# Performance work log

Measured on AMD Instinct MI355X. Metric: run time of the kernel, lower is better.

## Reference

```python
import jax, jax.numpy as jnp
import numpy as np

N_NODES = 50000
N_EDGES = 800000
D = 256


def gcn_conv(x, edge_index, W, b, n_nodes):
    """PyG-style GCNConv: add self-loops, symmetric norm, linear, scatter-add."""
    # add self loops
    loops = jnp.arange(n_nodes, dtype=edge_index.dtype)
    src = jnp.concatenate([edge_index[0], loops])  # message sources
    dst = jnp.concatenate([edge_index[1], loops])  # aggregation targets
    # symmetric normalization: deg computed on targets (incl. self loops)
    deg = jax.ops.segment_sum(jnp.ones_like(dst, dtype=x.dtype), dst,
                              num_segments=n_nodes)
    dinv = jnp.where(deg > 0, jax.lax.rsqrt(deg), 0.0)
    norm = dinv[src] * dinv[dst]  # [E+N]
    h = x @ W  # [N, out]
    msg = h[src] * norm[:, None]  # gather + scale, [E+N, out]
    out = jax.ops.segment_sum(msg, dst, num_segments=n_nodes)  # scatter-add
    return out + b


def setup_inputs() -> dict:
    key = jax.random.key(0)
    k1, k2, k3, k4 = jax.random.split(key, 4)
    x = jax.random.normal(k1, (N_NODES, D), dtype=jnp.float32)
    edge_index = jax.random.randint(k2, (2, N_EDGES), 0, N_NODES, dtype=jnp.int64)
    s = 1.0 / np.sqrt(D)
    W1 = jax.random.normal(k3, (D, D), dtype=jnp.float32) * s
    W2 = jax.random.normal(k4, (D, D), dtype=jnp.float32) * s
    b1 = jnp.zeros((D,), dtype=jnp.float32)
    b2 = jnp.zeros((D,), dtype=jnp.float32)
    return {"x": x, "edge_index": edge_index, "W1": W1, "b1": b1,
            "W2": W2, "b2": b2}


def reference(x, edge_index, W1, b1, W2, b2):
    n = x.shape[0]
    out = gcn_conv(x, edge_index, W1, b1, n)
    out = jax.nn.relu(out)  # dropout is identity in eval mode (p=0.2 in train)
    out = out + gcn_conv(x, edge_index, W2, b2, n)
    return out
```

## Files before the change

### kernel.cpp

```cpp
#include <hip/hip_runtime.h>
#include <hip/hip_bf16.h>

#define DIM 256
#define CAP 64
#define GEMM_BX 128

typedef short bf16x8 __attribute__((ext_vector_type(8)));
typedef float f32x4  __attribute__((ext_vector_type(4)));
typedef unsigned short u16x4 __attribute__((ext_vector_type(4)));

__device__ __forceinline__ unsigned short f2b(float f) {
    union { __hip_bfloat16 h; unsigned short u; } cv;
    cv.h = __float2bfloat16(f);
    return cv.u;
}
__device__ __forceinline__ float b2f(unsigned short u) {
    return __uint_as_float(((unsigned)u) << 16);
}
__device__ __forceinline__ void acc8(uint4 u, float* a) {
    a[0] += __uint_as_float(u.x << 16); a[1] += __uint_as_float(u.x & 0xffff0000u);
    a[2] += __uint_as_float(u.y << 16); a[3] += __uint_as_float(u.y & 0xffff0000u);
    a[4] += __uint_as_float(u.z << 16); a[5] += __uint_as_float(u.z & 0xffff0000u);
    a[6] += __uint_as_float(u.w << 16); a[7] += __uint_as_float(u.w & 0xffff0000u);
}

#define OFF_FILL   0
#define OFF_WT1    262144
#define OFF_WT2    393216
#define OFF_BUCKET 524288
#define OFF_AGG    6924544ull
#define OFF_YB     32524544ull
#define NEED_BF    (OFF_YB + 25600000ull)

__global__ void k_fill(const int* __restrict__ src, const int* __restrict__ dst,
                       int* __restrict__ fill, unsigned short* __restrict__ bucket, int nE) {
    int e = blockIdx.x * blockDim.x + threadIdx.x;
    if (e < nE) {
        int d = dst[e];
        int pos = atomicAdd(&fill[d], 1);
        if (pos < CAP) bucket[d * CAP + pos] = (unsigned short)src[e];
    }
}

__global__ void k_prep(const float* __restrict__ x, const int* __restrict__ fill,
                       uint4* __restrict__ yb,
                       const float* __restrict__ W1, const float* __restrict__ W2,
                       unsigned short* __restrict__ wt1, unsigned short* __restrict__ wt2,
                       int nybBlocks, int n8) {
    if ((int)blockIdx.x < nybBlocks) {
        int t = blockIdx.x * 256 + threadIdx.x;
        if (t < n8) {
            float d = rsqrtf((float)(1 + fill[t >> 5]));
            const f32x4* xp = (const f32x4*)x + t * 2;
            f32x4 v0 = xp[0], v1 = xp[1];
            uint4 r;
            r.x = (unsigned)f2b(d * v0.x) | ((unsigned)f2b(d * v0.y) << 16);
            r.y = (unsigned)f2b(d * v0.z) | ((unsigned)f2b(d * v0.w) << 16);
            r.z = (unsigned)f2b(d * v1.x) | ((unsigned)f2b(d * v1.y) << 16);
            r.w = (unsigned)f2b(d * v1.z) | ((unsigned)f2b(d * v1.w) << 16);
            yb[t] = r;
        }
    } else {
        int t = (blockIdx.x - nybBlocks) * 256 + threadIdx.x;
        if (t < DIM * DIM) {
            int k = t & 255, nn = t >> 8;
            wt1[t] = f2b(W1[k * DIM + nn]);
            wt2[t] = f2b(W2[k * DIM + nn]);
        }
    }
}

__global__ void k_agg_bf(const uint4* __restrict__ yb, const int* __restrict__ fill,
                         const unsigned short* __restrict__ bucket,
                         uint4* __restrict__ aggbf, int n) {
    int t    = blockIdx.x * blockDim.x + threadIdx.x;
    int wid  = t >> 6;
    int lane = threadIdx.x & 63;
    int node = wid * 2 + (lane >> 5);
    int h    = lane & 31;
    if (node >= n) return;

    float a[8];
    uint4 s = yb[(size_t)node * 32 + h];
#pragma unroll
    for (int i = 0; i < 8; i++) a[i] = 0.f;
    acc8(s, a);

    int c = fill[node];
    float di = rsqrtf((float)(1 + c));
    if (c > CAP) c = CAP;
    const unsigned short* bk = bucket + (size_t)node * CAP;

    int kfull = c & ~7;
    for (int k = 0; k < kfull; k += 8) {
        uint4 iv = *(const uint4*)(bk + k);
        int j0 = iv.x & 0xffff, j1 = iv.x >> 16;
        int j2 = iv.y & 0xffff, j3 = iv.y >> 16;
        int j4 = iv.z & 0xffff, j5 = iv.z >> 16;
        int j6 = iv.w & 0xffff, j7 = iv.w >> 16;
        uint4 r0 = yb[(size_t)j0 * 32 + h];
        uint4 r1 = yb[(size_t)j1 * 32 + h];
        uint4 r2 = yb[(size_t)j2 * 32 + h];
        uint4 r3 = yb[(size_t)j3 * 32 + h];
        uint4 r4 = yb[(size_t)j4 * 32 + h];
        uint4 r5 = yb[(size_t)j5 * 32 + h];
        uint4 r6 = yb[(size_t)j6 * 32 + h];
        uint4 r7 = yb[(size_t)j7 * 32 + h];
        acc8(r0, a); acc8(r1, a); acc8(r2, a); acc8(r3, a);
        acc8(r4, a); acc8(r5, a); acc8(r6, a); acc8(r7, a);
    }
    int rem = c - kfull;
    if (rem) {
        uint4 iv = *(const uint4*)(bk + kfull);
        int j0 = iv.x & 0xffff, j1 = iv.x >> 16;
        int j2 = iv.y & 0xffff, j3 = iv.y >> 16;
        int j4 = iv.z & 0xffff, j5 = iv.z >> 16;
        int j6 = iv.w & 0xffff;
        j1 = (rem > 1) ? j1 : 0;
        j2 = (rem > 2) ? j2 : 0;
        j3 = (rem > 3) ? j3 : 0;
        j4 = (rem > 4) ? j4 : 0;
        j5 = (rem > 5) ? j5 : 0;
        j6 = (rem > 6) ? j6 : 0;
        uint4 r0 = yb[(size_t)j0 * 32 + h];
        uint4 r1 = yb[(size_t)j1 * 32 + h];
        uint4 r2 = yb[(size_t)j2 * 32 + h];
        uint4 r3 = yb[(size_t)j3 * 32 + h];
        uint4 r4 = yb[(size_t)j4 * 32 + h];
        uint4 r5 = yb[(size_t)j5 * 32 + h];
        uint4 r6 = yb[(size_t)j6 * 32 + h];
        acc8(r0, a);
        if (rem > 1) acc8(r1, a);
        if (rem > 2) acc8(r2, a);
        if (rem > 3) acc8(r3, a);
        if (rem > 4) acc8(r4, a);
        if (rem > 5) acc8(r5, a);
        if (rem > 6) acc8(r6, a);
    }

    unsigned long long lo = (unsigned long long)((unsigned)f2b(a[0] * di) | ((unsigned)f2b(a[1] * di) << 16))
                          | ((unsigned long long)((unsigned)f2b(a[2] * di) | ((unsigned)f2b(a[3] * di) << 16)) << 32);
    unsigned long long hi = (unsigned long long)((unsigned)f2b(a[4] * di) | ((unsigned)f2b(a[5] * di) << 16))
                          | ((unsigned long long)((unsigned)f2b(a[6] * di) | ((unsigned)f2b(a[7] * di) << 16)) << 32);
    unsigned long long* dstp = (unsigned long long*)&aggbf[(size_t)node * 32 + h];
    __builtin_nontemporal_store(lo, dstp);
    __builtin_nontemporal_store(hi, dstp + 1);
}

__global__ void k_agg_f32(const float4* __restrict__ x4, const int* __restrict__ fill,
                          const unsigned short* __restrict__ bucket,
                          ushort4* __restrict__ aggbf, int n) {
    int node = (blockIdx.x * blockDim.x + threadIdx.x) >> 6;
    int lane = threadIdx.x & 63;
    if (node >= n) return;

    int c = fill[node];
    float di = rsqrtf((float)(1 + c));
    if (c > CAP) c = CAP;

    float4 xi = x4[(size_t)node * 64 + lane];
    float a0 = di * xi.x, a1 = di * xi.y, a2 = di * xi.z, a3 = di * xi.w;

    const unsigned short* bk = bucket + (size_t)node * CAP;
    for (int k = 0; k < c; k++) {
        int j = bk[k];
        float dj = rsqrtf((float)(1 + fill[j]));
        float4 xj = x4[(size_t)j * 64 + lane];
        a0 += dj * xj.x; a1 += dj * xj.y; a2 += dj * xj.z; a3 += dj * xj.w;
    }
    ushort4 r;
    r.x = f2b(a0 * di); r.y = f2b(a1 * di);
    r.z = f2b(a2 * di); r.w = f2b(a3 * di);
    aggbf[(size_t)node * 64 + lane] = r;
}

__launch_bounds__(256, 4)
__global__ void k_gemm(const short* __restrict__ aggbf,
                       const short* __restrict__ wt1, const short* __restrict__ wt2,
                       const float* __restrict__ b1, const float* __restrict__ b2,
                       float* __restrict__ out, int n, int ntiles) {
    __shared__ uint4 bs[4096];

    int c0  = blockIdx.y * 64;
    int tid = threadIdx.x;

#pragma unroll
    for (int i = 0; i < 16; i++) {
        int l = tid + i * 256;
        int m = l >> 11, rem = l & 2047, nn = rem >> 5, p = rem & 31;
        const short* base = (m == 0) ? wt1 : wt2;
        const uint4* sp = (const uint4*)(base + ((size_t)(c0 + nn)) * DIM) + p;
        bs[(m << 11) + (nn << 5) + (p ^ (nn & 31))] = *sp;
    }
    __syncthreads();

    int lane = tid & 63;
    int wave = tid >> 6;
    int lrow = lane & 15;
    int quad = lane >> 4;

    float bb1[4], bb2[4];
#pragma unroll
    for (int ct = 0; ct < 4; ct++) {
        bb1[ct] = b1[c0 + ct * 16 + lrow];
        bb2[ct] = b2[c0 + ct * 16 + lrow];
    }

    for (int t = blockIdx.x; t < ntiles; t += gridDim.x) {
        int rowbase = t * 128 + wave * 32;
        int r0 = rowbase + lrow;       if (r0 >= n) r0 = 0;
        int r1 = rowbase + 16 + lrow;  if (r1 >= n) r1 = 0;
        const short* ap0 = aggbf + (size_t)r0 * DIM + quad * 8;
        const short* ap1 = aggbf + (size_t)r1 * DIM + quad * 8;

        f32x4 acc1[2][4], acc2[2][4];
#pragma unroll
        for (int sub = 0; sub < 2; sub++)
#pragma unroll
            for (int ct = 0; ct < 4; ct++) {
                acc1[sub][ct] = (f32x4){0.f, 0.f, 0.f, 0.f};
                acc2[sub][ct] = (f32x4){0.f, 0.f, 0.f, 0.f};
            }

        bf16x8 a0 = *(const bf16x8*)(ap0);
        bf16x8 a1 = *(const bf16x8*)(ap1);
#pragma unroll
        for (int s = 0; s < 8; s++) {
            bf16x8 na0 = a0, na1 = a1;
            if (s < 7) {
                na0 = *(const bf16x8*)(ap0 + (s + 1) * 32);
                na1 = *(const bf16x8*)(ap1 + (s + 1) * 32);
            }
#pragma unroll
            for (int ct = 0; ct < 4; ct++) {
                int nn = ct * 16 + lrow;
                int ch = (4 * s + quad) ^ (nn & 31);
                uint4 u1 = bs[(nn << 5) + ch];
                uint4 u2 = bs[2048 + (nn << 5) + ch];
                bf16x8 w1f, w2f;
                __builtin_memcpy(&w1f, &u1, 16);
                __builtin_memcpy(&w2f, &u2, 16);
                acc1[0][ct] = __builtin_amdgcn_mfma_f32_16x16x32_bf16(a0, w1f, acc1[0][ct], 0, 0, 0);
                acc1[1][ct] = __builtin_amdgcn_mfma_f32_16x16x32_bf16(a1, w1f, acc1[1][ct], 0, 0, 0);
                acc2[0][ct] = __builtin_amdgcn_mfma_f32_16x16x32_bf16(a0, w2f, acc2[0][ct], 0, 0, 0);
                acc2[1][ct] = __builtin_amdgcn_mfma_f32_16x16x32_bf16(a1, w2f, acc2[1][ct], 0, 0, 0);
            }
            a0 = na0; a1 = na1;
        }

#pragma unroll
        for (int sub = 0; sub < 2; sub++) {
            int rb = rowbase + sub * 16 + quad * 4;
#pragma unroll
            for (int ct = 0; ct < 4; ct++) {
                int col = c0 + ct * 16 + lrow;
#pragma unroll
                for (int i = 0; i < 4; i++) {
                    int row = rb + i;
                    if (row < n) {
                        float v = fmaxf(acc1[sub][ct][i] + bb1[ct], 0.f)
                                + acc2[sub][ct][i] + bb2[ct];
                        __builtin_nontemporal_store(v, &out[(size_t)row * DIM + col]);
                    }
                }
            }
        }
    }
}

extern "C" void kernel_launch(void* const* d_in, const int* in_sizes, int n_in,
                              void* d_out, int out_size, void* d_ws, size_t ws_size,
                              hipStream_t stream) {
    const float* x  = (const float*)d_in[0];
    const int*   ei = (const int*)d_in[1];
    const float* W1 = (const float*)d_in[2];
    const float* b1 = (const float*)d_in[3];
    const float* W2 = (const float*)d_in[4];
    const float* b2 = (const float*)d_in[5];
    float* out = (float*)d_out;

    int n = in_sizes[0] / DIM;
    int E = in_sizes[1] / 2;
    const int* src = ei;
    const int* dst = ei + E;

    char* ws = (char*)d_ws;
    int*            fill   = (int*)(ws + OFF_FILL);
    unsigned short* wt1    = (unsigned short*)(ws + OFF_WT1);
    unsigned short* wt2    = (unsigned short*)(ws + OFF_WT2);
    unsigned short* bucket = (unsigned short*)(ws + OFF_BUCKET);
    char*           aggp   = ws + OFF_AGG;
    uint4*          yb     = (uint4*)(ws + OFF_YB);

    (void)hipMemsetAsync(fill, 0, n * sizeof(int), stream);

    k_fill<<<(E + 255) / 256, 256, 0, stream>>>(src, dst, fill, bucket, E);

    bool use_bf = (ws_size >= NEED_BF);
    if (use_bf) {
        int n8 = n * (DIM / 8);
        int nybBlocks = (n8 + 255) / 256;
        k_prep<<<nybBlocks + 256, 256, 0, stream>>>(x, fill, yb, W1, W2, wt1, wt2,
                                                    nybBlocks, n8);
        int aggBlocks = ((n + 1) / 2 * 64 + 255) / 256;
        k_agg_bf<<<aggBlocks, 256, 0, stream>>>(yb, fill, bucket, (uint4*)aggp, n);
    } else {
        k_prep<<<256, 256, 0, stream>>>(x, fill, yb, W1, W2, wt1, wt2, 0, 0);
        int aggBlocks = (n * 64 + 255) / 256;
        k_agg_f32<<<aggBlocks, 256, 0, stream>>>((const float4*)x, fill, bucket,
                                                 (ushort4*)aggp, n);
    }

    int ntiles = (n + 127) / 128;
    dim3 ggrid(GEMM_BX, DIM / 64);
    k_gemm<<<ggrid, 256, 0, stream>>>((const short*)aggp, (const short*)wt1,
                                      (const short*)wt2, b1, b2, out, n, ntiles);
}
```

Baseline: 256.0 us.

## Keep weight fragments in registers and swap MFMA operands for vectorized stores

The GEMM now gives each block a 32-column slice and loads all of that slice's W1/W2 bf16 fragments from LDS into registers once, instead of re-reading LDS inside every tile. The MFMA operands are swapped so each lane holds four consecutive output columns for one row, which allows 16-byte vector stores and vector bias loads in place of scalar stores. Tiles shrink to 64 rows, the grid becomes 64x8 blocks, and launch bounds drop to 2 blocks per SM to make room for the extra registers. In exchange, each aggregated row is re-read by twice as many column blocks, and occupancy may be lower.

```diff
diff --git a/kernel.cpp b/kernel.cpp
--- a/kernel.cpp
+++ b/kernel.cpp
@@ -3,7 +3,7 @@
 
 #define DIM 256
 #define CAP 64
-#define GEMM_BX 128
+#define GEMM_BX 64
 
 typedef short bf16x8 __attribute__((ext_vector_type(8)));
 typedef float f32x4  __attribute__((ext_vector_type(4)));
@@ -174,23 +174,23 @@
     aggbf[(size_t)node * 64 + lane] = r;
 }
 
-__launch_bounds__(256, 4)
+__launch_bounds__(256, 2)
 __global__ void k_gemm(const short* __restrict__ aggbf,
                        const short* __restrict__ wt1, const short* __restrict__ wt2,
                        const float* __restrict__ b1, const float* __restrict__ b2,
                        float* __restrict__ out, int n, int ntiles) {
-    __shared__ uint4 bs[4096];
-
-    int c0  = blockIdx.y * 64;
+    __shared__ uint4 bs[2048];
+
+    int c0  = blockIdx.y * 32;
     int tid = threadIdx.x;
 
 #pragma unroll
-    for (int i = 0; i < 16; i++) {
+    for (int i = 0; i < 8; i++) {
         int l = tid + i * 256;
-        int m = l >> 11, rem = l & 2047, nn = rem >> 5, p = rem & 31;
+        int m = l >> 10, rem = l & 1023, nn = rem >> 5, p = rem & 31;
         const short* base = (m == 0) ? wt1 : wt2;
-        const uint4* sp = (const uint4*)(base + ((size_t)(c0 + nn)) * DIM) + p;
-        bs[(m << 11) + (nn << 5) + (p ^ (nn & 31))] = *sp;
+        const uint4* sp = (const uint4*)(base + (size_t)(c0 + nn) * DIM) + p;
+        bs[(m << 10) + (nn << 5) + (p ^ nn)] = *sp;
     }
     __syncthreads();
 
@@ -199,70 +199,61 @@
     int lrow = lane & 15;
     int quad = lane >> 4;
 
-    float bb1[4], bb2[4];
-#pragma unroll
-    for (int ct = 0; ct < 4; ct++) {
-        bb1[ct] = b1[c0 + ct * 16 + lrow];
-        bb2[ct] = b2[c0 + ct * 16 + lrow];
+    bf16x8 w1r[2][8], w2r[2][8];
+#pragma unroll
+    for (int ct = 0; ct < 2; ct++) {
+        int nn = ct * 16 + lrow;
+#pragma unroll
+        for (int s = 0; s < 8; s++) {
+            int p = (4 * s + quad) ^ nn;
+            uint4 u = bs[(nn << 5) + p];
+            uint4 v = bs[1024 + (nn << 5) + p];
+            __builtin_memcpy(&w1r[ct][s], &u, 16);
+            __builtin_memcpy(&w2r[ct][s], &v, 16);
+        }
+    }
+
+    f32x4 bb1[2], bb2[2];
+#pragma unroll
+    for (int ct = 0; ct < 2; ct++) {
+        bb1[ct] = *(const f32x4*)&b1[c0 + ct * 16 + quad * 4];
+        bb2[ct] = *(const f32x4*)&b2[c0 + ct * 16 + quad * 4];
     }
 
     for (int t = blockIdx.x; t < ntiles; t += gridDim.x) {
-        int rowbase = t * 128 + wave * 32;
-        int r0 = rowbase + lrow;       if (r0 >= n) r0 = 0;
-        int r1 = rowbase + 16 + lrow;  if (r1 >= n) r1 = 0;
-        const short* ap0 = aggbf + (size_t)r0 * DIM + quad * 8;
-        const short* ap1 = aggbf + (size_t)r1 * DIM + quad * 8;
-
-        f32x4 acc1[2][4], acc2[2][4];
-#pragma unroll
-        for (int sub = 0; sub < 2; sub++)
-#pragma unroll
-            for (int ct = 0; ct < 4; ct++) {
-                acc1[sub][ct] = (f32x4){0.f, 0.f, 0.f, 0.f};
-                acc2[sub][ct] = (f32x4){0.f, 0.f, 0.f, 0.f};
+        int row = t * 64 + wave * 16 + lrow;
+        int r = (row < n) ? row : 0;
+        const short* ap = aggbf + (size_t)r * DIM + quad * 8;
+
+        bf16x8 A[8];
+#pragma unroll
+        for (int s = 0; s < 8; s++) A[s] = *(const bf16x8*)(ap + s * 32);
+
+        f32x4 acc1[2], acc2[2];
+#pragma unroll
+        for (int ct = 0; ct < 2; ct++) {
+            acc1[ct] = (f32x4){0.f, 0.f, 0.f, 0.f};
+            acc2[ct] = (f32x4){0.f, 0.f, 0.f, 0.f};
+        }
+
+#pragma unroll
+        for (int s = 0; s < 8; s++) {
+#pragma unroll
+            for (int ct = 0; ct < 2; ct++) {
+                acc1[ct] = __builtin_amdgcn_mfma_f32_16x16x32_bf16(w1r[ct][s], A[s], acc1[ct], 0, 0, 0);
+                acc2[ct] = __builtin_amdgcn_mfma_f32_16x16x32_bf16(w2r[ct][s], A[s], acc2[ct], 0, 0, 0);
             }
-
-        bf16x8 a0 = *(const bf16x8*)(ap0);
-        bf16x8 a1 = *(const bf16x8*)(ap1);
-#pragma unroll
-        for (int s = 0; s < 8; s++) {
-            bf16x8 na0 = a0, na1 = a1;
-            if (s < 7) {
-                na0 = *(const bf16x8*)(ap0 + (s + 1) * 32);
-                na1 = *(const bf16x8*)(ap1 + (s + 1) * 32);
-            }
-#pragma unroll
-            for (int ct = 0; ct < 4; ct++) {
-                int nn = ct * 16 + lrow;
-                int ch = (4 * s + quad) ^ (nn & 31);
-                uint4 u1 = bs[(nn << 5) + ch];
-                uint4 u2 = bs[2048 + (nn << 5) + ch];
-                bf16x8 w1f, w2f;
-                __builtin_memcpy(&w1f, &u1, 16);
-                __builtin_memcpy(&w2f, &u2, 16);
-                acc1[0][ct] = __builtin_amdgcn_mfma_f32_16x16x32_bf16(a0, w1f, acc1[0][ct], 0, 0, 0);
-                acc1[1][ct] = __builtin_amdgcn_mfma_f32_16x16x32_bf16(a1, w1f, acc1[1][ct], 0, 0, 0);
-                acc2[0][ct] = __builtin_amdgcn_mfma_f32_16x16x32_bf16(a0, w2f, acc2[0][ct], 0, 0, 0);
-                acc2[1][ct] = __builtin_amdgcn_mfma_f32_16x16x32_bf16(a1, w2f, acc2[1][ct], 0, 0, 0);
-            }
-            a0 = na0; a1 = na1;
-        }
-
-#pragma unroll
-        for (int sub = 0; sub < 2; sub++) {
-            int rb = rowbase + sub * 16 + quad * 4;
-#pragma unroll
-            for (int ct = 0; ct < 4; ct++) {
-                int col = c0 + ct * 16 + lrow;
-#pragma unroll
-                for (int i = 0; i < 4; i++) {
-                    int row = rb + i;
-                    if (row < n) {
-                        float v = fmaxf(acc1[sub][ct][i] + bb1[ct], 0.f)
-                                + acc2[sub][ct][i] + bb2[ct];
-                        __builtin_nontemporal_store(v, &out[(size_t)row * DIM + col]);
-                    }
-                }
+        }
+
+        if (row < n) {
+#pragma unroll
+            for (int ct = 0; ct < 2; ct++) {
+                f32x4 v;
+#pragma unroll
+                for (int i = 0; i < 4; i++)
+                    v[i] = fmaxf(acc1[ct][i] + bb1[ct][i], 0.f) + acc2[ct][i] + bb2[ct][i];
+                f32x4* dstp = (f32x4*)&out[(size_t)row * DIM + c0 + ct * 16 + quad * 4];
+                __builtin_nontemporal_store(v, dstp);
             }
         }
     }
@@ -311,8 +302,8 @@
                                                  (ushort4*)aggp, n);
     }
 
-    int ntiles = (n + 127) / 128;
-    dim3 ggrid(GEMM_BX, DIM / 64);
+    int ntiles = (n + 63) / 64;
+    dim3 ggrid(GEMM_BX, DIM / 32);
     k_gemm<<<ggrid, 256, 0, stream>>>((const short*)aggp, (const short*)wt1,
                                       (const short*)wt2, b1, b2, out, n, ntiles);
 }
```

Measured after the change: 242.9 us. -5.1%, faster.
